# Kernel optimization log

Hardware: AMD Instinct MI355X
Metric: run time of the kernel (lower is better)

Reference implementation:

```python
import jax, jax.numpy as jnp
import numpy as np


def setup_inputs() -> dict:
    key = jax.random.key(0)
    k1, k2 = jax.random.split(key)
    B, N, M, D = 4, 8192, 8192, 3
    prediction = jax.random.normal(k1, (B, N, D), dtype=jnp.float32)
    ground_truth = jax.random.normal(k2, (B, M, D), dtype=jnp.float32)
    return {"prediction": prediction, "ground_truth": ground_truth}


def reference(prediction, ground_truth):
    # Pairwise Euclidean distances via the expansion trick (avoids the
    x2 = jnp.sum(prediction * prediction, axis=-1)          # [B, N]
    y2 = jnp.sum(ground_truth * ground_truth, axis=-1)      # [B, M]
    xy = jnp.einsum('bnd,bmd->bnm', prediction, ground_truth)  # [B, N, M]
    d = jnp.sqrt(jnp.maximum(x2[..., :, None] + y2[..., None, :] - 2.0 * xy, 0.0))
    # Directed Hausdorff distances, then symmetric max.
    d_xy = jnp.max(jnp.min(d, axis=-1), axis=-1)  # max_n min_m  -> [B]
    d_yx = jnp.max(jnp.min(d, axis=-2), axis=-1)  # max_m min_n  -> [B]
    return jnp.maximum(d_xy, d_yx)
```

## Files before the change

kernel.cpp:

```cpp
#include <hip/hip_runtime.h>
#include <math.h>

#define BATCH 4
#define NPTS 8192
#define TB 256
#define NB 2
#define XW (NB * 32)
#define XSPAN (4 * XW)
#define XBLKS (NPTS / XSPAN)
#define YSPAN 1024
#define YBLKS (NPTS / YSPAN)
#define YTILES (YSPAN / 32)

typedef _Float16 f16x8 __attribute__((ext_vector_type(8)));
typedef float f32x16 __attribute__((ext_vector_type(16)));


__device__ __forceinline__ float tree17(f32x16 d, float r) {
    float v0 = fminf(fminf(d[0], d[1]), d[2]);
    float v1 = fminf(fminf(d[3], d[4]), d[5]);
    float v2 = fminf(fminf(d[6], d[7]), d[8]);
    float v3 = fminf(fminf(d[9], d[10]), d[11]);
    float v4 = fminf(fminf(d[12], d[13]), d[14]);
    float w0 = fminf(fminf(v0, v1), v2);
    float w1 = fminf(fminf(v3, v4), d[15]);
    return fminf(fminf(w0, w1), r);
}

#define MFMA2(D0, D1, AF)                                                     \
    asm volatile(                                                             \
        "s_nop 1\n\t"                                                         \
        "v_mfma_f32_32x32x16_f16 %0, %2, %3, %5\n\t"                          \
        "v_mfma_f32_32x32x16_f16 %1, %2, %4, %5\n\t"                          \
        "s_nop 7\n\t"                                                         \
        "s_nop 7\n\t"                                                         \
        "s_nop 1\n\t"                                                         \
        : "=&v"(D0), "=&v"(D1)                                                \
        : "v"(AF), "v"(bf0), "v"(bf1), "v"(zc));

__global__ __launch_bounds__(TB) void hd_mfma(const float* __restrict__ pred,
                                              const float* __restrict__ gt,
                                              unsigned* __restrict__ minbits) {
    const int tid = threadIdx.x;
    const int xblk = blockIdx.x % XBLKS;
    const int yblk = blockIdx.x / XBLKS;
    const int b = blockIdx.y;
    const int dir = blockIdx.z;

    const float* X = (dir == 0) ? pred + (size_t)b * NPTS * 3 : gt + (size_t)b * NPTS * 3;
    const float* Y = (dir == 0) ? gt + (size_t)b * NPTS * 3 : pred + (size_t)b * NPTS * 3;

    __shared__ __align__(16) _Float16 As[YSPAN * 16];

    const int ybase = yblk * YSPAN;
    for (int p = tid; p < YSPAN; p += TB) {
        int gp = ybase + p;
        float y0 = Y[3 * gp], y1 = Y[3 * gp + 1], y2 = Y[3 * gp + 2];
        _Float16 h0 = (_Float16)y0, h1 = (_Float16)y1, h2 = (_Float16)y2;
        _Float16 l0 = (_Float16)(y0 - (float)h0);
        _Float16 l1 = (_Float16)(y1 - (float)h1);
        _Float16 l2 = (_Float16)(y2 - (float)h2);
        float ys = fmaf(y0, y0, fmaf(y1, y1, y2 * y2));
        _Float16 sh = (_Float16)ys, sl = (_Float16)(ys - (float)sh);
        const _Float16 n2 = (_Float16)(-2.f);
        _Float16 A0 = n2 * h0, A1 = n2 * h1, A2 = n2 * h2;
        _Float16 C0 = n2 * l0, C1 = n2 * l1, C2 = n2 * l2;
        f16x8 g0 = {A0, A1, A2, A0, A1, A2, C0, C1};
        f16x8 g1 = {C2, C0, C1, C2, sh, sl, (_Float16)1.f, (_Float16)1.f};
        int t = p >> 5, q = p & 31;
        *(f16x8*)&As[t * 512 + q * 8] = g0;
        *(f16x8*)&As[t * 512 + 256 + q * 8] = g1;
    }

    const int wave = tid >> 6, lane = tid & 63, half = lane >> 5, ln = lane & 31;
    const int xw = xblk * XSPAN + wave * XW;
    f16x8 bf0, bf1;
#pragma unroll
    for (int i = 0; i < NB; ++i) {
        int px = xw + i * 32 + ln;
        float x0 = X[3 * px], x1 = X[3 * px + 1], x2 = X[3 * px + 2];
        _Float16 h0 = (_Float16)x0, h1 = (_Float16)x1, h2 = (_Float16)x2;
        _Float16 l0 = (_Float16)(x0 - (float)h0);
        _Float16 l1 = (_Float16)(x1 - (float)h1);
        _Float16 l2 = (_Float16)(x2 - (float)h2);
        float xs = fmaf(x0, x0, fmaf(x1, x1, x2 * x2));
        _Float16 sh = (_Float16)xs, sl = (_Float16)(xs - (float)sh);
        f16x8 g0 = {h0, h1, h2, l0, l1, l2, h0, h1};
        f16x8 g1 = {h2, l0, l1, l2, (_Float16)1.f, (_Float16)1.f, sh, sl};
        if (i == 0) bf0 = half ? g1 : g0;
        else        bf1 = half ? g1 : g0;
    }
    __syncthreads();

    const f32x16 zc = {0.f, 0.f, 0.f, 0.f, 0.f, 0.f, 0.f, 0.f,
                       0.f, 0.f, 0.f, 0.f, 0.f, 0.f, 0.f, 0.f};
    float rmin0 = 3.0e38f, rmin1 = 3.0e38f;

    int aoff = half * 256 + ln * 8;
    for (int u = 0; u < YTILES; ++u) {
        f16x8 af = *(const f16x8*)&As[aoff];
        aoff += 512;
        f32x16 d0, d1;
        MFMA2(d0, d1, af)
        rmin0 = tree17(d0, rmin0);
        rmin1 = tree17(d1, rmin1);
    }

    unsigned* mb = minbits + ((size_t)(dir * BATCH + b)) * NPTS;
    {
        float v = fminf(rmin0, __shfl_xor(rmin0, 32, 64));
        if (lane < 32) atomicMin(&mb[xw + ln], __float_as_uint(fmaxf(v, 0.f)));
    }
    {
        float v = fminf(rmin1, __shfl_xor(rmin1, 32, 64));
        if (lane < 32) atomicMin(&mb[xw + 32 + ln], __float_as_uint(fmaxf(v, 0.f)));
    }
}

__global__ __launch_bounds__(256) void hd_reduce(const unsigned* __restrict__ minbits,
                                                 float* __restrict__ out) {
    const int tid = threadIdx.x;
    const int b = blockIdx.x;
    const uint4* p0 = (const uint4*)(minbits + (size_t)b * NPTS);
    const uint4* p1 = (const uint4*)(minbits + (size_t)(BATCH + b) * NPTS);
    unsigned vmax = 0u;
    for (int i = tid; i < NPTS / 4; i += 256) {
        uint4 u = p0[i];
        uint4 v = p1[i];
        unsigned a = max(max(u.x, u.y), max(u.z, u.w));
        unsigned c = max(max(v.x, v.y), max(v.z, v.w));
        vmax = max(vmax, max(a, c));
    }
    __shared__ unsigned sm[256];
    sm[tid] = vmax;
    __syncthreads();
    for (int s = 128; s > 0; s >>= 1) {
        if (tid < s) sm[tid] = max(sm[tid], sm[tid + s]);
        __syncthreads();
    }
    if (tid == 0) out[b] = sqrtf(__uint_as_float(sm[0]));
}

extern "C" void kernel_launch(void* const* d_in, const int* in_sizes, int n_in,
                              void* d_out, int out_size, void* d_ws, size_t ws_size,
                              hipStream_t stream) {
    const float* pred = (const float*)d_in[0];
    const float* gt = (const float*)d_in[1];
    unsigned* minbits = (unsigned*)d_ws;

    (void)hipMemsetAsync(minbits, 0xFF, (size_t)2 * BATCH * NPTS * sizeof(unsigned),
                         stream);
    hd_mfma<<<dim3(XBLKS * YBLKS, BATCH, 2), TB, 0, stream>>>(pred, gt, minbits);
    hd_reduce<<<BATCH, 256, 0, stream>>>(minbits, (float*)d_out);
}
```

Baseline: 80.53 us.

## Use one MFMA per wave with smaller Y tiles and higher occupancy

Each wave now handles 32 query points instead of 64, issuing a single MFMA per Y tile rather than two back-to-back. The Y span per block is halved to 512 and launch bounds request 8 blocks per CU. This cuts per-wave register and shared memory use so more waves can hide the fixed s_nop MFMA latency padding. The cost is four times as many blocks, more Y-tile staging repeated across blocks, and more atomicMin traffic.

```diff
diff --git a/kernel.cpp b/kernel.cpp
--- a/kernel.cpp
+++ b/kernel.cpp
@@ -4,11 +4,10 @@
 #define BATCH 4
 #define NPTS 8192
 #define TB 256
-#define NB 2
-#define XW (NB * 32)
+#define XW 32
 #define XSPAN (4 * XW)
 #define XBLKS (NPTS / XSPAN)
-#define YSPAN 1024
+#define YSPAN 512
 #define YBLKS (NPTS / YSPAN)
 #define YTILES (YSPAN / 32)
 
@@ -27,20 +26,19 @@
     return fminf(fminf(w0, w1), r);
 }
 
-#define MFMA2(D0, D1, AF)                                                     \
+#define MFMA1(D0, AF, BF)                                                     \
     asm volatile(                                                             \
         "s_nop 1\n\t"                                                         \
-        "v_mfma_f32_32x32x16_f16 %0, %2, %3, %5\n\t"                          \
-        "v_mfma_f32_32x32x16_f16 %1, %2, %4, %5\n\t"                          \
+        "v_mfma_f32_32x32x16_f16 %0, %1, %2, %3\n\t"                          \
         "s_nop 7\n\t"                                                         \
         "s_nop 7\n\t"                                                         \
         "s_nop 1\n\t"                                                         \
-        : "=&v"(D0), "=&v"(D1)                                                \
-        : "v"(AF), "v"(bf0), "v"(bf1), "v"(zc));
+        : "=&v"(D0)                                                           \
+        : "v"(AF), "v"(BF), "v"(zc));
 
-__global__ __launch_bounds__(TB) void hd_mfma(const float* __restrict__ pred,
-                                              const float* __restrict__ gt,
-                                              unsigned* __restrict__ minbits) {
+__global__ __launch_bounds__(TB, 8) void hd_mfma(const float* __restrict__ pred,
+                                                 const float* __restrict__ gt,
+                                                 unsigned* __restrict__ minbits) {
     const int tid = threadIdx.x;
     const int xblk = blockIdx.x % XBLKS;
     const int yblk = blockIdx.x / XBLKS;
@@ -74,10 +72,9 @@
 
     const int wave = tid >> 6, lane = tid & 63, half = lane >> 5, ln = lane & 31;
     const int xw = xblk * XSPAN + wave * XW;
-    f16x8 bf0, bf1;
-#pragma unroll
-    for (int i = 0; i < NB; ++i) {
-        int px = xw + i * 32 + ln;
+    f16x8 bf0;
+    {
+        int px = xw + ln;
         float x0 = X[3 * px], x1 = X[3 * px + 1], x2 = X[3 * px + 2];
         _Float16 h0 = (_Float16)x0, h1 = (_Float16)x1, h2 = (_Float16)x2;
         _Float16 l0 = (_Float16)(x0 - (float)h0);
@@ -87,33 +84,27 @@
         _Float16 sh = (_Float16)xs, sl = (_Float16)(xs - (float)sh);
         f16x8 g0 = {h0, h1, h2, l0, l1, l2, h0, h1};
         f16x8 g1 = {h2, l0, l1, l2, (_Float16)1.f, (_Float16)1.f, sh, sl};
-        if (i == 0) bf0 = half ? g1 : g0;
-        else        bf1 = half ? g1 : g0;
+        bf0 = half ? g1 : g0;
     }
     __syncthreads();
 
     const f32x16 zc = {0.f, 0.f, 0.f, 0.f, 0.f, 0.f, 0.f, 0.f,
                        0.f, 0.f, 0.f, 0.f, 0.f, 0.f, 0.f, 0.f};
-    float rmin0 = 3.0e38f, rmin1 = 3.0e38f;
+    float rmin0 = 3.0e38f;
 
     int aoff = half * 256 + ln * 8;
     for (int u = 0; u < YTILES; ++u) {
         f16x8 af = *(const f16x8*)&As[aoff];
         aoff += 512;
-        f32x16 d0, d1;
-        MFMA2(d0, d1, af)
+        f32x16 d0;
+        MFMA1(d0, af, bf0)
         rmin0 = tree17(d0, rmin0);
-        rmin1 = tree17(d1, rmin1);
     }
 
     unsigned* mb = minbits + ((size_t)(dir * BATCH + b)) * NPTS;
     {
         float v = fminf(rmin0, __shfl_xor(rmin0, 32, 64));
         if (lane < 32) atomicMin(&mb[xw + ln], __float_as_uint(fmaxf(v, 0.f)));
-    }
-    {
-        float v = fminf(rmin1, __shfl_xor(rmin1, 32, 64));
-        if (lane < 32) atomicMin(&mb[xw + 32 + ln], __float_as_uint(fmaxf(v, 0.f)));
     }
 }
 
```

Result: no change. 80.32 us (-0.3%).

## Fuse min-reduction and final max into one kernel with per-block Y sweep

Applied to the files above, without the earlier changes.

Each block now owns 64 X points and sweeps over all Y points in 512-point LDS chunks, with the four waves splitting each chunk's tiles. Per-point minima are combined across waves in shared memory, and the block's max is atomically merged into the output. This removes the separate reduce kernel, the large per-point min workspace with its memset, and the per-point global atomicMin traffic. In exchange, every block re-converts all of Y, which is about four times more preprocessing in total. The launch also has half as many blocks and two barriers per small chunk, which may hurt MFMA overlap.

```diff
diff --git a/kernel.cpp b/kernel.cpp
--- a/kernel.cpp
+++ b/kernel.cpp
@@ -4,13 +4,11 @@
 #define BATCH 4
 #define NPTS 8192
 #define TB 256
-#define NB 2
-#define XW (NB * 32)
-#define XSPAN (4 * XW)
+#define XSPAN 64
 #define XBLKS (NPTS / XSPAN)
-#define YSPAN 1024
-#define YBLKS (NPTS / YSPAN)
-#define YTILES (YSPAN / 32)
+#define CH 512
+#define NCH (NPTS / CH)
+#define TPC (CH / 32)
 
 typedef _Float16 f16x8 __attribute__((ext_vector_type(8)));
 typedef float f32x16 __attribute__((ext_vector_type(16)));
@@ -27,7 +25,7 @@
     return fminf(fminf(w0, w1), r);
 }
 
-#define MFMA2(D0, D1, AF)                                                     \
+#define MFMA2(D0, D1, AF, BFa, BFb)                                           \
     asm volatile(                                                             \
         "s_nop 1\n\t"                                                         \
         "v_mfma_f32_32x32x16_f16 %0, %2, %3, %5\n\t"                          \
@@ -36,47 +34,27 @@
         "s_nop 7\n\t"                                                         \
         "s_nop 1\n\t"                                                         \
         : "=&v"(D0), "=&v"(D1)                                                \
-        : "v"(AF), "v"(bf0), "v"(bf1), "v"(zc));
+        : "v"(AF), "v"(BFa), "v"(BFb), "v"(zc));
 
-__global__ __launch_bounds__(TB) void hd_mfma(const float* __restrict__ pred,
-                                              const float* __restrict__ gt,
-                                              unsigned* __restrict__ minbits) {
+__global__ __launch_bounds__(TB) void hd_one(const float* __restrict__ pred,
+                                             const float* __restrict__ gt,
+                                             unsigned* __restrict__ outbits) {
     const int tid = threadIdx.x;
-    const int xblk = blockIdx.x % XBLKS;
-    const int yblk = blockIdx.x / XBLKS;
+    const int xblk = blockIdx.x;
     const int b = blockIdx.y;
     const int dir = blockIdx.z;
 
     const float* X = (dir == 0) ? pred + (size_t)b * NPTS * 3 : gt + (size_t)b * NPTS * 3;
     const float* Y = (dir == 0) ? gt + (size_t)b * NPTS * 3 : pred + (size_t)b * NPTS * 3;
 
-    __shared__ __align__(16) _Float16 As[YSPAN * 16];
-
-    const int ybase = yblk * YSPAN;
-    for (int p = tid; p < YSPAN; p += TB) {
-        int gp = ybase + p;
-        float y0 = Y[3 * gp], y1 = Y[3 * gp + 1], y2 = Y[3 * gp + 2];
-        _Float16 h0 = (_Float16)y0, h1 = (_Float16)y1, h2 = (_Float16)y2;
-        _Float16 l0 = (_Float16)(y0 - (float)h0);
-        _Float16 l1 = (_Float16)(y1 - (float)h1);
-        _Float16 l2 = (_Float16)(y2 - (float)h2);
-        float ys = fmaf(y0, y0, fmaf(y1, y1, y2 * y2));
-        _Float16 sh = (_Float16)ys, sl = (_Float16)(ys - (float)sh);
-        const _Float16 n2 = (_Float16)(-2.f);
-        _Float16 A0 = n2 * h0, A1 = n2 * h1, A2 = n2 * h2;
-        _Float16 C0 = n2 * l0, C1 = n2 * l1, C2 = n2 * l2;
-        f16x8 g0 = {A0, A1, A2, A0, A1, A2, C0, C1};
-        f16x8 g1 = {C2, C0, C1, C2, sh, sl, (_Float16)1.f, (_Float16)1.f};
-        int t = p >> 5, q = p & 31;
-        *(f16x8*)&As[t * 512 + q * 8] = g0;
-        *(f16x8*)&As[t * 512 + 256 + q * 8] = g1;
-    }
+    __shared__ __align__(16) _Float16 As[CH * 16];
+    __shared__ float pmin[4][XSPAN];
 
     const int wave = tid >> 6, lane = tid & 63, half = lane >> 5, ln = lane & 31;
-    const int xw = xblk * XSPAN + wave * XW;
+    const int xw = xblk * XSPAN;
     f16x8 bf0, bf1;
 #pragma unroll
-    for (int i = 0; i < NB; ++i) {
+    for (int i = 0; i < 2; ++i) {
         int px = xw + i * 32 + ln;
         float x0 = X[3 * px], x1 = X[3 * px + 1], x2 = X[3 * px + 2];
         _Float16 h0 = (_Float16)x0, h1 = (_Float16)x1, h2 = (_Float16)x2;
@@ -90,55 +68,63 @@
         if (i == 0) bf0 = half ? g1 : g0;
         else        bf1 = half ? g1 : g0;
     }
-    __syncthreads();
 
     const f32x16 zc = {0.f, 0.f, 0.f, 0.f, 0.f, 0.f, 0.f, 0.f,
                        0.f, 0.f, 0.f, 0.f, 0.f, 0.f, 0.f, 0.f};
     float rmin0 = 3.0e38f, rmin1 = 3.0e38f;
 
-    int aoff = half * 256 + ln * 8;
-    for (int u = 0; u < YTILES; ++u) {
-        f16x8 af = *(const f16x8*)&As[aoff];
-        aoff += 512;
-        f32x16 d0, d1;
-        MFMA2(d0, d1, af)
-        rmin0 = tree17(d0, rmin0);
-        rmin1 = tree17(d1, rmin1);
+    for (int c = 0; c < NCH; ++c) {
+        const int ybase = c * CH;
+        for (int p = tid; p < CH; p += TB) {
+            int gp = ybase + p;
+            float y0 = Y[3 * gp], y1 = Y[3 * gp + 1], y2 = Y[3 * gp + 2];
+            _Float16 h0 = (_Float16)y0, h1 = (_Float16)y1, h2 = (_Float16)y2;
+            _Float16 l0 = (_Float16)(y0 - (float)h0);
+            _Float16 l1 = (_Float16)(y1 - (float)h1);
+            _Float16 l2 = (_Float16)(y2 - (float)h2);
+            float ys = fmaf(y0, y0, fmaf(y1, y1, y2 * y2));
+            _Float16 sh = (_Float16)ys, sl = (_Float16)(ys - (float)sh);
+            const _Float16 n2 = (_Float16)(-2.f);
+            _Float16 A0 = n2 * h0, A1 = n2 * h1, A2 = n2 * h2;
+            _Float16 C0 = n2 * l0, C1 = n2 * l1, C2 = n2 * l2;
+            f16x8 g0 = {A0, A1, A2, A0, A1, A2, C0, C1};
+            f16x8 g1 = {C2, C0, C1, C2, sh, sl, (_Float16)1.f, (_Float16)1.f};
+            int t = p >> 5, q = p & 31;
+            *(f16x8*)&As[t * 512 + q * 8] = g0;
+            *(f16x8*)&As[t * 512 + 256 + q * 8] = g1;
+        }
+        __syncthreads();
+
+#pragma unroll
+        for (int j = 0; j < 4; ++j) {
+            int t = wave * 4 + j;
+            f16x8 af = *(const f16x8*)&As[t * 512 + half * 256 + ln * 8];
+            f32x16 d0, d1;
+            MFMA2(d0, d1, af, bf0, bf1)
+            rmin0 = tree17(d0, rmin0);
+            rmin1 = tree17(d1, rmin1);
+        }
+        __syncthreads();
     }
 
-    unsigned* mb = minbits + ((size_t)(dir * BATCH + b)) * NPTS;
     {
-        float v = fminf(rmin0, __shfl_xor(rmin0, 32, 64));
-        if (lane < 32) atomicMin(&mb[xw + ln], __float_as_uint(fmaxf(v, 0.f)));
+        float v0 = fminf(rmin0, __shfl_xor(rmin0, 32, 64));
+        float v1 = fminf(rmin1, __shfl_xor(rmin1, 32, 64));
+        if (lane < 32) {
+            pmin[wave][ln] = v0;
+            pmin[wave][32 + ln] = v1;
+        }
     }
-    {
-        float v = fminf(rmin1, __shfl_xor(rmin1, 32, 64));
-        if (lane < 32) atomicMin(&mb[xw + 32 + ln], __float_as_uint(fmaxf(v, 0.f)));
+    __syncthreads();
+    if (tid < 64) {
+        float m = fminf(fminf(pmin[0][tid], pmin[1][tid]),
+                        fminf(pmin[2][tid], pmin[3][tid]));
+        m = fmaxf(m, 0.f);
+#pragma unroll
+        for (int off = 32; off > 0; off >>= 1)
+            m = fmaxf(m, __shfl_xor(m, off, 64));
+        if (tid == 0) atomicMax(&outbits[b], __float_as_uint(sqrtf(m)));
     }
-}
-
-__global__ __launch_bounds__(256) void hd_reduce(const unsigned* __restrict__ minbits,
-                                                 float* __restrict__ out) {
-    const int tid = threadIdx.x;
-    const int b = blockIdx.x;
-    const uint4* p0 = (const uint4*)(minbits + (size_t)b * NPTS);
-    const uint4* p1 = (const uint4*)(minbits + (size_t)(BATCH + b) * NPTS);
-    unsigned vmax = 0u;
-    for (int i = tid; i < NPTS / 4; i += 256) {
-        uint4 u = p0[i];
-        uint4 v = p1[i];
-        unsigned a = max(max(u.x, u.y), max(u.z, u.w));
-        unsigned c = max(max(v.x, v.y), max(v.z, v.w));
-        vmax = max(vmax, max(a, c));
-    }
-    __shared__ unsigned sm[256];
-    sm[tid] = vmax;
-    __syncthreads();
-    for (int s = 128; s > 0; s >>= 1) {
-        if (tid < s) sm[tid] = max(sm[tid], sm[tid + s]);
-        __syncthreads();
-    }
-    if (tid == 0) out[b] = sqrtf(__uint_as_float(sm[0]));
 }
 
 extern "C" void kernel_launch(void* const* d_in, const int* in_sizes, int n_in,
@@ -146,10 +132,7 @@
                               hipStream_t stream) {
     const float* pred = (const float*)d_in[0];
     const float* gt = (const float*)d_in[1];
-    unsigned* minbits = (unsigned*)d_ws;
 
-    (void)hipMemsetAsync(minbits, 0xFF, (size_t)2 * BATCH * NPTS * sizeof(unsigned),
-                         stream);
-    hd_mfma<<<dim3(XBLKS * YBLKS, BATCH, 2), TB, 0, stream>>>(pred, gt, minbits);
-    hd_reduce<<<BATCH, 256, 0, stream>>>(minbits, (float*)d_out);
+    (void)hipMemsetAsync(d_out, 0, (size_t)out_size * sizeof(float), stream);
+    hd_one<<<dim3(XBLKS, BATCH, 2), TB, 0, stream>>>(pred, gt, (unsigned*)d_out);
 }
```

Measured after the change: 86.17 us. +7.0%, slower.
